# Kernel optimization log

Measured on AMD Instinct MI355X. Metric: run time of the kernel, lower is better.

## Reference

```python
import jax, jax.numpy as jnp
import numpy as np

N_NODES = 50000
DIM = 128
N_EDGES = 800000
N_UID = 4096
ORDER = 3
LN_EPS = 1e-5


def setup_inputs() -> dict:
    key = jax.random.key(0)
    ks = jax.random.split(key, 6)
    scale = 1.0 / np.sqrt(DIM)
    embedding = jax.random.normal(ks[0], (N_NODES, DIM), jnp.float32) * np.sqrt(2.0 / DIM)  # kaiming-ish
    W = jax.random.normal(ks[1], (ORDER, DIM, DIM), jnp.float32) * scale
    b = jnp.zeros((ORDER, DIM), jnp.float32)
    gamma = jnp.ones((ORDER, DIM), jnp.float32)
    beta = jnp.zeros((ORDER, DIM), jnp.float32)
    src = jax.random.randint(ks[2], (N_EDGES,), 0, N_NODES, jnp.int32)
    dst = jax.random.randint(ks[3], (N_EDGES,), 0, N_NODES, jnp.int32)
    uid = jax.random.randint(ks[4], (N_UID,), 0, N_NODES, jnp.int32)
    return {"embedding": embedding, "W": W, "b": b, "gamma": gamma,
            "beta": beta, "src": src, "dst": dst, "uid": uid}


def _layer_norm(x, g, bta):
    mu = jnp.mean(x, axis=-1, keepdims=True)
    var = jnp.var(x, axis=-1, keepdims=True)
    return (x - mu) * jax.lax.rsqrt(var + LN_EPS) * g + bta


def reference(embedding, W, b, gamma, beta, src, dst, uid):
    # in-degree per destination node (DGL 'gcn' aggregator uses in_degrees)
    deg = jax.ops.segment_sum(jnp.ones((src.shape[0],), embedding.dtype), dst,
                              num_segments=N_NODES)  # [N]
    inv = (1.0 / (deg + 1.0))[:, None]  # [N,1]
    feats = embedding
    for i in range(ORDER):
        # gather source features, scatter-sum into destinations
        neigh = jax.ops.segment_sum(feats[src], dst, num_segments=N_NODES)  # [N,D]
        h = (neigh + feats) * inv                    # gcn-style mean incl. self
        h = jnp.einsum('nd,ed->ne', h, W[i]) + b[i]  # fc_neigh
        feats = jax.nn.elu(_layer_norm(h, gamma[i], beta[i]))
    return feats[uid]  # [N_UID, D]
```

## Files before the change

### kernel.cpp

```cpp
#include <hip/hip_runtime.h>
#include <math.h>

typedef unsigned int   uint;
typedef unsigned short ushort;

#define N_NODES 50000
#define DIM     128
#define N_EDGES 800000
#define N_UID   4096
#define LN_EPS  1e-5f
#define RST     132
#define NBUCK   196
#define PCHUNK  4096

typedef __attribute__((ext_vector_type(8))) short bf16x8;
typedef __attribute__((ext_vector_type(4))) float f32x4;
typedef __attribute__((ext_vector_type(2))) float f32x2;
typedef __attribute__((ext_vector_type(4))) uint  u32x4;

__device__ __forceinline__ float bf_lo(uint u) { return __builtin_bit_cast(float, u << 16); }
__device__ __forceinline__ float bf_hi(uint u) { return __builtin_bit_cast(float, u & 0xffff0000u); }
__device__ __forceinline__ uint pack_bf16(float a, float b) {
    uint ua = __builtin_bit_cast(uint, a);
    uint ub = __builtin_bit_cast(uint, b);
    uint ra = (ua + 0x7fffu + ((ua >> 16) & 1u)) >> 16;
    uint rb = (ub + 0x7fffu + ((ub >> 16) & 1u)) >> 16;
    return ra | (rb << 16);
}

__global__ __launch_bounds__(256) void prep_kernel(const float* __restrict__ emb, ushort* __restrict__ E,
                                                   const float* __restrict__ W, ushort* __restrict__ WB,
                                                   int* __restrict__ bhist,
                                                   ushort* __restrict__ T1, ushort* __restrict__ T2) {
    int i = blockIdx.x * 256 + threadIdx.x;
    if (i < N_NODES * DIM / 4) {
        const float4 v = ((const float4*)emb)[i];
        uint2 p;
        p.x = pack_bf16(v.x, v.y);
        p.y = pack_bf16(v.z, v.w);
        ((uint2*)E)[i] = p;
    }
    if (i < 3 * DIM * DIM / 4) {
        const float4 v = ((const float4*)W)[i];
        uint2 p;
        p.x = pack_bf16(v.x, v.y);
        p.y = pack_bf16(v.z, v.w);
        ((uint2*)WB)[i] = p;
    }
    if (i < NBUCK) bhist[i] = 0;
    if (i < DIM / 4) {
        const uint2 z = make_uint2(0u, 0u);
        ((uint2*)(E  + (size_t)N_NODES * DIM))[i] = z;
        ((uint2*)(T1 + (size_t)N_NODES * DIM))[i] = z;
        ((uint2*)(T2 + (size_t)N_NODES * DIM))[i] = z;
    }
}

__global__ __launch_bounds__(256) void bhist_kernel(const int* __restrict__ dst, int* __restrict__ bhist) {
    __shared__ int h[256];
    const int t = threadIdx.x;
    h[t] = 0;
    __syncthreads();
    for (int e = blockIdx.x * 256 + t; e < N_EDGES; e += gridDim.x * 256)
        atomicAdd(&h[dst[e] >> 8], 1);
    __syncthreads();
    if (t < NBUCK && h[t]) atomicAdd(&bhist[t], h[t]);
}

__global__ __launch_bounds__(256) void bscan_kernel(const int* __restrict__ bhist, int* __restrict__ bbase,
                                                    int* __restrict__ bcur, int* __restrict__ off) {
    __shared__ int sh[256];
    const int t = threadIdx.x;
    const int v = (t < NBUCK) ? bhist[t] : 0;
    sh[t] = v;
    __syncthreads();
    for (int o = 1; o < 256; o <<= 1) {
        int x = (t >= o) ? sh[t - o] : 0;
        __syncthreads();
        sh[t] += x;
        __syncthreads();
    }
    const int excl = sh[t] - v;
    if (t < NBUCK) { bbase[t] = excl; bcur[t] = excl; }
    if (t == NBUCK - 1) bbase[NBUCK] = excl + v;
    if (t == 0) off[N_NODES] = N_EDGES;
}

__global__ __launch_bounds__(256) void part_kernel(const int* __restrict__ src, const int* __restrict__ dst,
                                                   int* __restrict__ bcur, int2* __restrict__ pak) {
    __shared__ int h[256];
    __shared__ int base[256];
    __shared__ int cur[256];
    const int t  = threadIdx.x;
    const int e0 = blockIdx.x * PCHUNK;
    const int e1 = min(e0 + PCHUNK, N_EDGES);
    h[t] = 0;
    __syncthreads();
    for (int i = e0 + t; i < e1; i += 256)
        atomicAdd(&h[dst[i] >> 8], 1);
    __syncthreads();
    if (t < NBUCK && h[t]) base[t] = atomicAdd(&bcur[t], h[t]);
    cur[t] = 0;
    __syncthreads();
    for (int i = e0 + t; i < e1; i += 256) {
        const int s = src[i], d = dst[i];
        const int b = d >> 8;
        const int q = atomicAdd(&cur[b], 1);
        pak[base[b] + q] = make_int2(s, d);
    }
}

__global__ __launch_bounds__(256) void bucket_kernel(const int2* __restrict__ pak, const int* __restrict__ bbase,
                                                     int* __restrict__ off, int* __restrict__ csr) {
    __shared__ int cnt[256];
    __shared__ int pos[256];
    const int b = blockIdx.x, t = threadIdx.x;
    const int e0 = bbase[b], e1 = bbase[b + 1], m = e1 - e0;
    cnt[t] = 0;
    __syncthreads();
    for (int i = t; i < m; i += 256) atomicAdd(&cnt[pak[e0 + i].y & 255], 1);
    __syncthreads();
    const int v = cnt[t];
    pos[t] = v;
    __syncthreads();
    for (int o = 1; o < 256; o <<= 1) {
        int x = (t >= o) ? pos[t - o] : 0;
        __syncthreads();
        pos[t] += x;
        __syncthreads();
    }
    const int excl = pos[t] - v;
    const int node = b * 256 + t;
    if (node < N_NODES) off[node] = e0 + excl;
    __syncthreads();
    pos[t] = excl;
    __syncthreads();
    for (int i = t; i < m; i += 256) {
        const int2 p = pak[e0 + i];
        const int q = atomicAdd(&pos[p.y & 255], 1);
        csr[e0 + q] = p.x;
    }
}

__global__ __launch_bounds__(256) void agg_kernel(
    const ushort* __restrict__ fin, ushort* __restrict__ xm,
    const int* __restrict__ off, const int* __restrict__ csr,
    const int* __restrict__ uidmap, int nrows)
{
    const int t    = threadIdx.x;
    const int lx   = t & 15;
    const int st   = t >> 4;
    const int slot = blockIdx.x * 16 + st;
    if (slot >= nrows) return;
    const int n = uidmap ? uidmap[slot] : slot;

    const uint4 q0 = ((const uint4*)(fin + (size_t)n * DIM))[lx];
    const int d0 = off[n];
    const int d1 = off[n + 1];
    const int deg = d1 - d0;

    f32x2 a[4];
    a[0] = f32x2{bf_lo(q0.x), bf_hi(q0.x)};
    a[1] = f32x2{bf_lo(q0.y), bf_hi(q0.y)};
    a[2] = f32x2{bf_lo(q0.z), bf_hi(q0.z)};
    a[3] = f32x2{bf_lo(q0.w), bf_hi(q0.w)};

    const int rounds = (deg + 7) >> 3;
    int id[8];
    int e = d0;
    if (rounds > 0) {
        #pragma unroll
        for (int k = 0; k < 8; ++k) {
            const int ee = e + k;
            const int c = csr[ee];
            id[k] = (ee < d1) ? c : N_NODES;
        }
    }
    for (int r = 0; r < rounds; ++r) {
        uint4 v[8];
        #pragma unroll
        for (int k = 0; k < 8; ++k)
            v[k] = ((const uint4*)(fin + (size_t)id[k] * DIM))[lx];
        if (r + 1 < rounds) {
            #pragma unroll
            for (int k = 0; k < 8; ++k) {
                const int ee = e + 8 + k;
                const int c = csr[ee];
                id[k] = (ee < d1) ? c : N_NODES;
            }
        }
        #pragma unroll
        for (int k = 0; k < 8; ++k) {
            a[0] += f32x2{bf_lo(v[k].x), bf_hi(v[k].x)};
            a[1] += f32x2{bf_lo(v[k].y), bf_hi(v[k].y)};
            a[2] += f32x2{bf_lo(v[k].z), bf_hi(v[k].z)};
            a[3] += f32x2{bf_lo(v[k].w), bf_hi(v[k].w)};
        }
        e += 8;
    }

    const float iv = 1.0f / (float)(deg + 1);
    uint4 p;
    p.x = pack_bf16(a[0].x * iv, a[0].y * iv);
    p.y = pack_bf16(a[1].x * iv, a[1].y * iv);
    p.z = pack_bf16(a[2].x * iv, a[2].y * iv);
    p.w = pack_bf16(a[3].x * iv, a[3].y * iv);
    *((uint4*)(xm + (size_t)slot * DIM + lx * 8)) = p;
}

template <bool OUT_BF16>
__global__ __launch_bounds__(512) void gemmln_kernel(
    const ushort* xm, void* fout,
    const ushort* __restrict__ wb, const float* __restrict__ bias,
    const float* __restrict__ gamma, const float* __restrict__ beta, int nrows)
{
    __shared__ float ys[32 * RST];
    const int t = threadIdx.x;
    const int rows = blockIdx.x * 32;

    {
        const int wave = t >> 6, lane = t & 63;
        const int row_off = (wave >> 2) * 16;
        const int col_off = (wave & 3) * 32;
        const int lm   = lane & 15;
        const int quad = lane >> 4;
        const int arow = min(rows + row_off + lm, nrows - 1);
        const ushort* xrow = xm + (size_t)arow * DIM + quad * 8;
        const ushort* wrow = wb + (size_t)(col_off + lm) * DIM + quad * 8;
        f32x4 acc[2] = {f32x4{0,0,0,0}, f32x4{0,0,0,0}};
        #pragma unroll
        for (int kk = 0; kk < 4; ++kk) {
            const bf16x8 af = __builtin_bit_cast(bf16x8, *(const u32x4*)(xrow + kk * 32));
            #pragma unroll
            for (int c = 0; c < 2; ++c) {
                const bf16x8 bfr = __builtin_bit_cast(bf16x8,
                    *(const u32x4*)(wrow + (size_t)c * 16 * DIM + kk * 32));
                acc[c] = __builtin_amdgcn_mfma_f32_16x16x32_bf16(af, bfr, acc[c], 0, 0, 0);
            }
        }
        #pragma unroll
        for (int c = 0; c < 2; ++c) {
            #pragma unroll
            for (int r = 0; r < 4; ++r)
                ys[(row_off + quad * 4 + r) * RST + col_off + c * 16 + lm] = acc[c][r];
        }
    }
    __syncthreads();

    {
        const int r   = t >> 4;
        const int seg = t & 15;
        const int db  = seg * 8;
        const float* yr = ys + r * RST + db;
        float vs[8];
        {
            const float4 y0 = ((const float4*)yr)[0];
            const float4 y1 = ((const float4*)yr)[1];
            const float4 b0 = ((const float4*)(bias + db))[0];
            const float4 b1 = ((const float4*)(bias + db))[1];
            vs[0] = y0.x + b0.x; vs[1] = y0.y + b0.y; vs[2] = y0.z + b0.z; vs[3] = y0.w + b0.w;
            vs[4] = y1.x + b1.x; vs[5] = y1.y + b1.y; vs[6] = y1.z + b1.z; vs[7] = y1.w + b1.w;
        }
        float s1 = 0.0f, s2 = 0.0f;
        #pragma unroll
        for (int i = 0; i < 8; ++i) { s1 += vs[i]; s2 += vs[i] * vs[i]; }
        #pragma unroll
        for (int m = 1; m < 16; m <<= 1) {
            s1 += __shfl_xor(s1, m);
            s2 += __shfl_xor(s2, m);
        }
        const float mu  = s1 * (1.0f / 128.0f);
        const float var = s2 * (1.0f / 128.0f) - mu * mu;
        const float rs  = rsqrtf(var + LN_EPS);
        float ov[8];
        {
            const float4 g0 = ((const float4*)(gamma + db))[0];
            const float4 g1 = ((const float4*)(gamma + db))[1];
            const float4 t0 = ((const float4*)(beta + db))[0];
            const float4 t1 = ((const float4*)(beta + db))[1];
            float z;
            z = (vs[0] - mu) * rs * g0.x + t0.x; ov[0] = (z > 0.0f) ? z : __expf(z) - 1.0f;
            z = (vs[1] - mu) * rs * g0.y + t0.y; ov[1] = (z > 0.0f) ? z : __expf(z) - 1.0f;
            z = (vs[2] - mu) * rs * g0.z + t0.z; ov[2] = (z > 0.0f) ? z : __expf(z) - 1.0f;
            z = (vs[3] - mu) * rs * g0.w + t0.w; ov[3] = (z > 0.0f) ? z : __expf(z) - 1.0f;
            z = (vs[4] - mu) * rs * g1.x + t1.x; ov[4] = (z > 0.0f) ? z : __expf(z) - 1.0f;
            z = (vs[5] - mu) * rs * g1.y + t1.y; ov[5] = (z > 0.0f) ? z : __expf(z) - 1.0f;
            z = (vs[6] - mu) * rs * g1.z + t1.z; ov[6] = (z > 0.0f) ? z : __expf(z) - 1.0f;
            z = (vs[7] - mu) * rs * g1.w + t1.w; ov[7] = (z > 0.0f) ? z : __expf(z) - 1.0f;
        }
        const int n = rows + r;
        if (n < nrows) {
            if (OUT_BF16) {
                uint4 p;
                p.x = pack_bf16(ov[0], ov[1]);
                p.y = pack_bf16(ov[2], ov[3]);
                p.z = pack_bf16(ov[4], ov[5]);
                p.w = pack_bf16(ov[6], ov[7]);
                *((uint4*)((ushort*)fout + (size_t)n * DIM + db)) = p;
            } else {
                float* op = (float*)fout + (size_t)n * DIM + db;
                ((float4*)op)[0] = make_float4(ov[0], ov[1], ov[2], ov[3]);
                ((float4*)op)[1] = make_float4(ov[4], ov[5], ov[6], ov[7]);
            }
        }
    }
}

extern "C" void kernel_launch(void* const* d_in, const int* in_sizes, int n_in,
                              void* d_out, int out_size, void* d_ws, size_t ws_size,
                              hipStream_t stream) {
    const float* emb   = (const float*)d_in[0];
    const float* W     = (const float*)d_in[1];
    const float* bias  = (const float*)d_in[2];
    const float* gamma = (const float*)d_in[3];
    const float* beta  = (const float*)d_in[4];
    const int*   src   = (const int*)d_in[5];
    const int*   dst   = (const int*)d_in[6];
    const int*   uid   = (const int*)d_in[7];

    const size_t FROW = (size_t)(N_NODES + 1) * DIM;
    ushort* E    = (ushort*)d_ws;
    ushort* T1   = E + FROW;
    ushort* T2   = T1 + FROW;
    ushort* WB   = T2 + FROW;
    int*    off  = (int*)(WB + 3 * DIM * DIM);
    int*    bhist = off + (N_NODES + 4);
    int*    bbase = bhist + 256;
    int*    bcur  = bbase + 260;
    int2*   pak   = (int2*)(bcur + 256);
    int*    csr   = (int*)(pak + N_EDGES);

    prep_kernel<<<(N_NODES * DIM / 4 + 255) / 256, 256, 0, stream>>>(emb, E, W, WB, bhist, T1, T2);
    bhist_kernel<<<512, 256, 0, stream>>>(dst, bhist);
    bscan_kernel<<<1, 256, 0, stream>>>(bhist, bbase, bcur, off);
    part_kernel<<<(N_EDGES + PCHUNK - 1) / PCHUNK, 256, 0, stream>>>(src, dst, bcur, pak);
    bucket_kernel<<<NBUCK, 256, 0, stream>>>(pak, bbase, off, csr);

    const int ablk = N_NODES / 16;
    const int gblk = (N_NODES + 31) / 32;

    agg_kernel<<<ablk, 256, 0, stream>>>(E, T1, off, csr, nullptr, N_NODES);
    gemmln_kernel<true><<<gblk, 512, 0, stream>>>(T1, T1, WB, bias, gamma, beta, N_NODES);
    agg_kernel<<<ablk, 256, 0, stream>>>(T1, T2, off, csr, nullptr, N_NODES);
    gemmln_kernel<true><<<gblk, 512, 0, stream>>>(T2, T2, WB + DIM * DIM,
                                                  bias + DIM, gamma + DIM, beta + DIM, N_NODES);
    agg_kernel<<<N_UID / 16, 256, 0, stream>>>(T2, T1, off, csr, uid, N_UID);
    gemmln_kernel<false><<<N_UID / 32, 512, 0, stream>>>(T1, (float*)d_out, WB + 2 * DIM * DIM,
                                                         bias + 2 * DIM, gamma + 2 * DIM,
                                                         beta + 2 * DIM, N_UID);
}
```

Baseline: 245.1 us.

## Fuse aggregation with GEMM+LN and restrict layer 2 to uid receptive field

Merges the gather-aggregate and GEMM/LayerNorm/ELU stages into one kernel that keeps the aggregated rows in shared memory instead of writing and rereading them. Layer 2 now runs only on the uid nodes and their in-neighbours, collected by new mark and compact kernels, since only those rows feed the final output. Edge packing is also shrunk to one int per edge. This costs extra small kernels and an atomic-based worklist, and layer 2 launches a full-size grid that exits early past the dynamic count.

Result: faster. 231.4 us (-5.6%).

```diff
diff --git a/kernel.cpp b/kernel.cpp
--- a/kernel.cpp
+++ b/kernel.cpp
@@ -10,6 +10,7 @@
 #define N_UID   4096
 #define LN_EPS  1e-5f
 #define RST     132
+#define XST     136
 #define NBUCK   196
 #define PCHUNK  4096
 
@@ -31,7 +32,8 @@
 __global__ __launch_bounds__(256) void prep_kernel(const float* __restrict__ emb, ushort* __restrict__ E,
                                                    const float* __restrict__ W, ushort* __restrict__ WB,
                                                    int* __restrict__ bhist,
-                                                   ushort* __restrict__ T1, ushort* __restrict__ T2) {
+                                                   ushort* __restrict__ T1, ushort* __restrict__ T2,
+                                                   int* __restrict__ mark, int* __restrict__ cnt) {
     int i = blockIdx.x * 256 + threadIdx.x;
     if (i < N_NODES * DIM / 4) {
         const float4 v = ((const float4*)emb)[i];
@@ -48,6 +50,8 @@
         ((uint2*)WB)[i] = p;
     }
     if (i < NBUCK) bhist[i] = 0;
+    if (i < N_NODES) mark[i] = 0;
+    if (i == 0) cnt[0] = 0;
     if (i < DIM / 4) {
         const uint2 z = make_uint2(0u, 0u);
         ((uint2*)(E  + (size_t)N_NODES * DIM))[i] = z;
@@ -87,7 +91,7 @@
 }
 
 __global__ __launch_bounds__(256) void part_kernel(const int* __restrict__ src, const int* __restrict__ dst,
-                                                   int* __restrict__ bcur, int2* __restrict__ pak) {
+                                                   int* __restrict__ bcur, int* __restrict__ pak) {
     __shared__ int h[256];
     __shared__ int base[256];
     __shared__ int cur[256];
@@ -106,11 +110,11 @@
         const int s = src[i], d = dst[i];
         const int b = d >> 8;
         const int q = atomicAdd(&cur[b], 1);
-        pak[base[b] + q] = make_int2(s, d);
-    }
-}
-
-__global__ __launch_bounds__(256) void bucket_kernel(const int2* __restrict__ pak, const int* __restrict__ bbase,
+        pak[base[b] + q] = (s << 8) | (d & 255);
+    }
+}
+
+__global__ __launch_bounds__(256) void bucket_kernel(const int* __restrict__ pak, const int* __restrict__ bbase,
                                                      int* __restrict__ off, int* __restrict__ csr) {
     __shared__ int cnt[256];
     __shared__ int pos[256];
@@ -118,7 +122,7 @@
     const int e0 = bbase[b], e1 = bbase[b + 1], m = e1 - e0;
     cnt[t] = 0;
     __syncthreads();
-    for (int i = t; i < m; i += 256) atomicAdd(&cnt[pak[e0 + i].y & 255], 1);
+    for (int i = t; i < m; i += 256) atomicAdd(&cnt[pak[e0 + i] & 255], 1);
     __syncthreads();
     const int v = cnt[t];
     pos[t] = v;
@@ -136,87 +140,105 @@
     pos[t] = excl;
     __syncthreads();
     for (int i = t; i < m; i += 256) {
-        const int2 p = pak[e0 + i];
-        const int q = atomicAdd(&pos[p.y & 255], 1);
-        csr[e0 + q] = p.x;
-    }
-}
-
-__global__ __launch_bounds__(256) void agg_kernel(
-    const ushort* __restrict__ fin, ushort* __restrict__ xm,
+        const int p = pak[e0 + i];
+        const int q = atomicAdd(&pos[p & 255], 1);
+        csr[e0 + q] = p >> 8;
+    }
+}
+
+__global__ __launch_bounds__(256) void mark_kernel(const int* __restrict__ uid, const int* __restrict__ off,
+                                                   const int* __restrict__ csr, int* __restrict__ mark) {
+    const int i = blockIdx.x * 256 + threadIdx.x;
+    if (i >= N_UID) return;
+    const int n = uid[i];
+    mark[n] = 1;
+    const int d0 = off[n], d1 = off[n + 1];
+    for (int e = d0; e < d1; ++e) mark[csr[e]] = 1;
+}
+
+__global__ __launch_bounds__(256) void compact_kernel(const int* __restrict__ mark, int* __restrict__ wl,
+                                                      int* __restrict__ cnt) {
+    const int i = blockIdx.x * 256 + threadIdx.x;
+    if (i < N_NODES && mark[i]) wl[atomicAdd(cnt, 1)] = i;
+}
+
+template <bool OUT_BF16, bool OUT_BY_NODE>
+__global__ __launch_bounds__(512) void layer_kernel(
+    const ushort* __restrict__ fin, void* __restrict__ fout,
     const int* __restrict__ off, const int* __restrict__ csr,
-    const int* __restrict__ uidmap, int nrows)
+    const int* __restrict__ uidmap, const ushort* __restrict__ wb,
+    const float* __restrict__ bias, const float* __restrict__ gamma,
+    const float* __restrict__ beta, int nrows, const int* __restrict__ nrows_dyn)
 {
-    const int t    = threadIdx.x;
-    const int lx   = t & 15;
-    const int st   = t >> 4;
-    const int slot = blockIdx.x * 16 + st;
-    if (slot >= nrows) return;
-    const int n = uidmap ? uidmap[slot] : slot;
-
-    const uint4 q0 = ((const uint4*)(fin + (size_t)n * DIM))[lx];
-    const int d0 = off[n];
-    const int d1 = off[n + 1];
-    const int deg = d1 - d0;
-
-    f32x2 a[4];
-    a[0] = f32x2{bf_lo(q0.x), bf_hi(q0.x)};
-    a[1] = f32x2{bf_lo(q0.y), bf_hi(q0.y)};
-    a[2] = f32x2{bf_lo(q0.z), bf_hi(q0.z)};
-    a[3] = f32x2{bf_lo(q0.w), bf_hi(q0.w)};
-
-    const int rounds = (deg + 7) >> 3;
-    int id[8];
-    int e = d0;
-    if (rounds > 0) {
-        #pragma unroll
-        for (int k = 0; k < 8; ++k) {
-            const int ee = e + k;
-            const int c = csr[ee];
-            id[k] = (ee < d1) ? c : N_NODES;
-        }
-    }
-    for (int r = 0; r < rounds; ++r) {
-        uint4 v[8];
-        #pragma unroll
-        for (int k = 0; k < 8; ++k)
-            v[k] = ((const uint4*)(fin + (size_t)id[k] * DIM))[lx];
-        if (r + 1 < rounds) {
+    __shared__ ushort xs[32 * XST];
+    __shared__ float  ys[32 * RST];
+    const int t = threadIdx.x;
+    const int nr = nrows_dyn ? *nrows_dyn : nrows;
+    const int rows = blockIdx.x * 32;
+    if (rows >= nr) return;
+
+    {
+        const int lx   = t & 15;
+        const int st   = t >> 4;
+        const int slot = rows + st;
+        const bool valid = slot < nr;
+        int n = 0;
+        if (valid) n = uidmap ? uidmap[slot] : slot;
+        const uint4 q0 = ((const uint4*)(fin + (size_t)n * DIM))[lx];
+        const int d0 = off[n];
+        int d1 = off[n + 1];
+        if (!valid) d1 = d0;
+        const int deg = d1 - d0;
+
+        f32x2 a[4];
+        a[0] = f32x2{bf_lo(q0.x), bf_hi(q0.x)};
+        a[1] = f32x2{bf_lo(q0.y), bf_hi(q0.y)};
+        a[2] = f32x2{bf_lo(q0.z), bf_hi(q0.z)};
+        a[3] = f32x2{bf_lo(q0.w), bf_hi(q0.w)};
+
+        const int rounds = (deg + 7) >> 3;
+        int id[8];
+        int e = d0;
+        if (rounds > 0) {
             #pragma unroll
             for (int k = 0; k < 8; ++k) {
-                const int ee = e + 8 + k;
+                const int ee = e + k;
                 const int c = csr[ee];
                 id[k] = (ee < d1) ? c : N_NODES;
             }
         }
-        #pragma unroll
-        for (int k = 0; k < 8; ++k) {
-            a[0] += f32x2{bf_lo(v[k].x), bf_hi(v[k].x)};
-            a[1] += f32x2{bf_lo(v[k].y), bf_hi(v[k].y)};
-            a[2] += f32x2{bf_lo(v[k].z), bf_hi(v[k].z)};
-            a[3] += f32x2{bf_lo(v[k].w), bf_hi(v[k].w)};
-        }
-        e += 8;
-    }
-
-    const float iv = 1.0f / (float)(deg + 1);
-    uint4 p;
-    p.x = pack_bf16(a[0].x * iv, a[0].y * iv);
-    p.y = pack_bf16(a[1].x * iv, a[1].y * iv);
-    p.z = pack_bf16(a[2].x * iv, a[2].y * iv);
-    p.w = pack_bf16(a[3].x * iv, a[3].y * iv);
-    *((uint4*)(xm + (size_t)slot * DIM + lx * 8)) = p;
-}
-
-template <bool OUT_BF16>
-__global__ __launch_bounds__(512) void gemmln_kernel(
-    const ushort* xm, void* fout,
-    const ushort* __restrict__ wb, const float* __restrict__ bias,
-    const float* __restrict__ gamma, const float* __restrict__ beta, int nrows)
-{
-    __shared__ float ys[32 * RST];
-    const int t = threadIdx.x;
-    const int rows = blockIdx.x * 32;
+        for (int r = 0; r < rounds; ++r) {
+            uint4 v[8];
+            #pragma unroll
+            for (int k = 0; k < 8; ++k)
+                v[k] = ((const uint4*)(fin + (size_t)id[k] * DIM))[lx];
+            if (r + 1 < rounds) {
+                #pragma unroll
+                for (int k = 0; k < 8; ++k) {
+                    const int ee = e + 8 + k;
+                    const int c = csr[ee];
+                    id[k] = (ee < d1) ? c : N_NODES;
+                }
+            }
+            #pragma unroll
+            for (int k = 0; k < 8; ++k) {
+                a[0] += f32x2{bf_lo(v[k].x), bf_hi(v[k].x)};
+                a[1] += f32x2{bf_lo(v[k].y), bf_hi(v[k].y)};
+                a[2] += f32x2{bf_lo(v[k].z), bf_hi(v[k].z)};
+                a[3] += f32x2{bf_lo(v[k].w), bf_hi(v[k].w)};
+            }
+            e += 8;
+        }
+
+        const float iv = 1.0f / (float)(deg + 1);
+        uint4 p;
+        p.x = pack_bf16(a[0].x * iv, a[0].y * iv);
+        p.y = pack_bf16(a[1].x * iv, a[1].y * iv);
+        p.z = pack_bf16(a[2].x * iv, a[2].y * iv);
+        p.w = pack_bf16(a[3].x * iv, a[3].y * iv);
+        *((uint4*)(xs + st * XST + lx * 8)) = p;
+    }
+    __syncthreads();
 
     {
         const int wave = t >> 6, lane = t & 63;
@@ -224,10 +246,9 @@
         const int col_off = (wave & 3) * 32;
         const int lm   = lane & 15;
         const int quad = lane >> 4;
-        const int arow = min(rows + row_off + lm, nrows - 1);
-        const ushort* xrow = xm + (size_t)arow * DIM + quad * 8;
-        const ushort* wrow = wb + (size_t)(col_off + lm) * DIM + quad * 8;
         f32x4 acc[2] = {f32x4{0,0,0,0}, f32x4{0,0,0,0}};
+        const ushort* xrow = xs + (row_off + lm) * XST + quad * 8;
+        const ushort* __restrict__ wrow = wb + (size_t)(col_off + lm) * DIM + quad * 8;
         #pragma unroll
         for (int kk = 0; kk < 4; ++kk) {
             const bf16x8 af = __builtin_bit_cast(bf16x8, *(const u32x4*)(xrow + kk * 32));
@@ -288,17 +309,18 @@
             z = (vs[6] - mu) * rs * g1.z + t1.z; ov[6] = (z > 0.0f) ? z : __expf(z) - 1.0f;
             z = (vs[7] - mu) * rs * g1.w + t1.w; ov[7] = (z > 0.0f) ? z : __expf(z) - 1.0f;
         }
-        const int n = rows + r;
-        if (n < nrows) {
+        const int slot = rows + r;
+        if (slot < nr) {
+            const int orow = OUT_BY_NODE ? uidmap[slot] : slot;
             if (OUT_BF16) {
                 uint4 p;
                 p.x = pack_bf16(ov[0], ov[1]);
                 p.y = pack_bf16(ov[2], ov[3]);
                 p.z = pack_bf16(ov[4], ov[5]);
                 p.w = pack_bf16(ov[6], ov[7]);
-                *((uint4*)((ushort*)fout + (size_t)n * DIM + db)) = p;
+                *((uint4*)((ushort*)fout + (size_t)orow * DIM + db)) = p;
             } else {
-                float* op = (float*)fout + (size_t)n * DIM + db;
+                float* op = (float*)fout + (size_t)orow * DIM + db;
                 ((float4*)op)[0] = make_float4(ov[0], ov[1], ov[2], ov[3]);
                 ((float4*)op)[1] = make_float4(ov[4], ov[5], ov[6], ov[7]);
             }
@@ -327,25 +349,29 @@
     int*    bhist = off + (N_NODES + 4);
     int*    bbase = bhist + 256;
     int*    bcur  = bbase + 260;
-    int2*   pak   = (int2*)(bcur + 256);
-    int*    csr   = (int*)(pak + N_EDGES);
-
-    prep_kernel<<<(N_NODES * DIM / 4 + 255) / 256, 256, 0, stream>>>(emb, E, W, WB, bhist, T1, T2);
+    int*    mark  = bcur + 256;
+    int*    wl    = mark + N_NODES;
+    int*    cnt   = wl + N_NODES;
+    int*    pak   = cnt + 4;
+    int*    csr   = pak + N_EDGES;
+
+    prep_kernel<<<(N_NODES * DIM / 4 + 255) / 256, 256, 0, stream>>>(emb, E, W, WB, bhist, T1, T2, mark, cnt);
     bhist_kernel<<<512, 256, 0, stream>>>(dst, bhist);
     bscan_kernel<<<1, 256, 0, stream>>>(bhist, bbase, bcur, off);
     part_kernel<<<(N_EDGES + PCHUNK - 1) / PCHUNK, 256, 0, stream>>>(src, dst, bcur, pak);
     bucket_kernel<<<NBUCK, 256, 0, stream>>>(pak, bbase, off, csr);
-
-    const int ablk = N_NODES / 16;
-    const int gblk = (N_NODES + 31) / 32;
-
-    agg_kernel<<<ablk, 256, 0, stream>>>(E, T1, off, csr, nullptr, N_NODES);
-    gemmln_kernel<true><<<gblk, 512, 0, stream>>>(T1, T1, WB, bias, gamma, beta, N_NODES);
-    agg_kernel<<<ablk, 256, 0, stream>>>(T1, T2, off, csr, nullptr, N_NODES);
-    gemmln_kernel<true><<<gblk, 512, 0, stream>>>(T2, T2, WB + DIM * DIM,
-                                                  bias + DIM, gamma + DIM, beta + DIM, N_NODES);
-    agg_kernel<<<N_UID / 16, 256, 0, stream>>>(T2, T1, off, csr, uid, N_UID);
-    gemmln_kernel<false><<<N_UID / 32, 512, 0, stream>>>(T1, (float*)d_out, WB + 2 * DIM * DIM,
-                                                         bias + 2 * DIM, gamma + 2 * DIM,
-                                                         beta + 2 * DIM, N_UID);
-}
+    mark_kernel<<<(N_UID + 255) / 256, 256, 0, stream>>>(uid, off, csr, mark);
+    compact_kernel<<<(N_NODES + 255) / 256, 256, 0, stream>>>(mark, wl, cnt);
+
+    const int lblk = (N_NODES + 31) / 32;
+
+    layer_kernel<true, false><<<lblk, 512, 0, stream>>>(E, T1, off, csr, nullptr, WB,
+                                                        bias, gamma, beta, N_NODES, nullptr);
+    layer_kernel<true, true><<<lblk, 512, 0, stream>>>(T1, T2, off, csr, wl, WB + DIM * DIM,
+                                                       bias + DIM, gamma + DIM, beta + DIM,
+                                                       0, cnt);
+    layer_kernel<false, false><<<N_UID / 32, 512, 0, stream>>>(T2, (float*)d_out, off, csr, uid,
+                                                               WB + 2 * DIM * DIM, bias + 2 * DIM,
+                                                               gamma + 2 * DIM, beta + 2 * DIM,
+                                                               N_UID, nullptr);
+}
```
